# Optimization experiments

Measured on AMD Instinct MI355X. Metric: run time of the kernel, lower is better.

Reference implementation:

```python
import jax, jax.numpy as jnp
import numpy as np

N, E, H, C = 10000, 160000, 7, 64
NEG_SLOPE = 0.2


def setup_inputs() -> dict:
    key = jax.random.key(0)
    ks = iter(jax.random.split(key, 32))
    def w(shape, fan_in):
        return jax.random.normal(next(ks), shape, jnp.float32) * (1.0 / np.sqrt(fan_in))
    inp = {
        "x": jax.random.normal(next(ks), (N, 1024), jnp.float32),
        "edge_index": jax.random.randint(next(ks), (2, E), 0, N, jnp.int64),
        # input MLP 1024->512->256->64
        "W1": w((1024, 512), 1024), "b1": jnp.zeros((512,), jnp.float32),
        "W2": w((512, 256), 512),   "b2": jnp.zeros((256,), jnp.float32),
        "W3": w((256, 64), 256),    "b3": jnp.zeros((64,), jnp.float32),
        # 5 stacked GATv2Conv(64,64,heads=7,concat=False) layers
        "Wl": w((5, 64, H * C), 64), "bl": jnp.zeros((5, H * C), jnp.float32),
        "Wr": w((5, 64, H * C), 64),
        "att": w((5, H, C), C),
        "cbias": jnp.zeros((5, C), jnp.float32),
        # output MLP 64->32->16->9
        "V1": w((64, 32), 64), "c1": jnp.zeros((32,), jnp.float32),
        "V2": w((32, 16), 32), "c2": jnp.zeros((16,), jnp.float32),
        "V3": w((16, 9), 16),  "c3": jnp.zeros((9,), jnp.float32),
    }
    return inp


def _gatv2_conv(x, src, dst, Wl, bl, Wr, att, bias):
    # x: [N,64]; src/dst: [E'] (self-loops already appended)
    xl = (x @ Wl + bl).reshape(N, H, C)   # lin_l (with bias)
    xr = (x @ Wr).reshape(N, H, C)        # lin_r (no bias)
    e = jax.nn.leaky_relu(xl[src] + xr[dst], NEG_SLOPE)      # [E',H,C]
    logits = jnp.einsum('ehc,hc->eh', e, att)                # [E',H]
    m = jax.ops.segment_max(logits, dst, num_segments=N)     # [N,H]
    a = jnp.exp(logits - m[dst])
    s = jax.ops.segment_sum(a, dst, num_segments=N)          # [N,H]
    alpha = a / (s[dst] + 1e-16)                             # ragged softmax per dst node
    out = jax.ops.segment_sum(alpha[:, :, None] * xl[src], dst, num_segments=N)  # [N,H,C]
    return out.mean(axis=1) + bias                           # concat=False -> mean heads


def reference(x, edge_index, W1, b1, W2, b2, W3, b3, Wl, bl, Wr, att, cbias,
              V1, c1, V2, c2, V3, c3):
    # GATv2Conv adds self-loops by default
    loops = jnp.arange(N, dtype=edge_index.dtype)
    src = jnp.concatenate([edge_index[0], loops])
    dst = jnp.concatenate([edge_index[1], loops])

    h = jax.nn.relu(x @ W1 + b1)
    h = jax.nn.relu(h @ W2 + b2)
    h = jax.nn.relu(h @ W3 + b3)
    for l in range(5):
        h = jax.nn.relu(_gatv2_conv(h, src, dst, Wl[l], bl[l], Wr[l], att[l], cbias[l]))
    h = jax.nn.relu(h) @ V1 + c1
    h = jax.nn.relu(h) @ V2 + c2
    h = jax.nn.relu(h) @ V3 + c3
    return jax.nn.log_softmax(h, axis=1)
```

## Files before the change

### kernel.cpp

```cpp
#include <hip/hip_runtime.h>
#include <hip/hip_bf16.h>
#include <math.h>

#define NNODES 10000
#define NEDGES 160000
#define ETOT (NEDGES + NNODES)
#define HEADS 7
#define CH 64
#define HC 448
#define HCP 1024

typedef __attribute__((ext_vector_type(8))) short short8;
typedef __attribute__((ext_vector_type(4))) float floatx4;

__device__ __forceinline__ float bf_lo(unsigned u) {
  return __uint_as_float(u << 16);
}
__device__ __forceinline__ float bf_hi(unsigned u) {
  return __uint_as_float(u & 0xffff0000u);
}

__global__ __launch_bounds__(256) void convert_f32_bf16(
    const float* __restrict__ in, short* __restrict__ out, int n4) {
  int i = blockIdx.x * 256 + threadIdx.x;
  if (i < n4) {
    float4 v = *(const float4*)&in[(size_t)i * 4];
    short4 o;
    o.x = __bfloat16_as_short(__float2bfloat16(v.x));
    o.y = __bfloat16_as_short(__float2bfloat16(v.y));
    o.z = __bfloat16_as_short(__float2bfloat16(v.z));
    o.w = __bfloat16_as_short(__float2bfloat16(v.w));
    *(short4*)&out[(size_t)i * 4] = o;
  }
}

__global__ __launch_bounds__(256) void transpose_bf16(
    const float* __restrict__ in, short* __restrict__ out, int K, int N) {
  int idx = blockIdx.x * 256 + threadIdx.x;
  if (idx < K * N) {
    int n = idx / K, k = idx % K;
    out[idx] = __bfloat16_as_short(__float2bfloat16(in[(size_t)k * N + n]));
  }
}

__global__ __launch_bounds__(256) void pack_gat(
    const float* __restrict__ Wl, const float* __restrict__ Wr,
    const float* __restrict__ bl, short* __restrict__ Wgt,
    float* __restrict__ bg) {
  int idx = blockIdx.x * 256 + threadIdx.x;
  if (idx < 5 * HCP * 64) {
    int l = idx / (HCP * 64);
    int rem = idx % (HCP * 64);
    int col = rem / 64, k = rem % 64;
    int half = col >> 9;
    int within = col & 511;
    int c = within >> 3, h = within & 7;
    float v = 0.f;
    if (h < 7) {
      const float* W = half ? Wr : Wl;
      v = W[((size_t)l * 64 + k) * HC + h * 64 + c];
    }
    Wgt[idx] = __bfloat16_as_short(__float2bfloat16(v));
  }
  if (idx < 5 * HCP) {
    int l = idx >> 10, col = idx & 1023;
    int half = col >> 9, within = col & 511;
    int c = within >> 3, h = within & 7;
    bg[idx] = (!half && h < 7) ? bl[(size_t)l * HC + h * 64 + c] : 0.f;
  }
}

template <int BM, int BN, int RELU>
__global__ __launch_bounds__(256) void mfma_gemm(
    const short* __restrict__ A, const short* __restrict__ Bt,
    const float* __restrict__ bias, short* __restrict__ C,
    int M, int K, int Nc) {
  __shared__ short As[BM * 64];
  __shared__ short Bs[BN * 64];
  constexpr int MI = BM / 32;
  constexpr int NJ = BN / 32;
  int tid = threadIdx.x;
  int lane = tid & 63, wave = tid >> 6;
  int wm = wave >> 1, wn = wave & 1;
  int row0 = blockIdx.x * BM, col0 = blockIdx.y * BN;
  floatx4 acc[MI][NJ] = {};

  for (int k0 = 0; k0 < K; k0 += 64) {
    #pragma unroll
    for (int i = 0; i < BM / 32; ++i) {
      int c = i * 4 + wave;
      int r = c * 8 + (lane >> 3);
      int k = (lane & 7) * 8;
      int grow = row0 + r;
      if (grow >= M) grow = M - 1;
      __builtin_amdgcn_global_load_lds(
          (const __attribute__((address_space(1))) void*)(A + (size_t)grow * K + k0 + k),
          (__attribute__((address_space(3))) void*)(As + c * 512), 16, 0, 0);
    }
    #pragma unroll
    for (int i = 0; i < BN / 32; ++i) {
      int c = i * 4 + wave;
      int r = c * 8 + (lane >> 3);
      int k = (lane & 7) * 8;
      int gcol = col0 + r;
      if (gcol >= Nc) gcol = Nc - 1;
      __builtin_amdgcn_global_load_lds(
          (const __attribute__((address_space(1))) void*)(Bt + (size_t)gcol * K + k0 + k),
          (__attribute__((address_space(3))) void*)(Bs + c * 512), 16, 0, 0);
    }
    __syncthreads();
    int lr = lane & 15, lq = lane >> 4;
    #pragma unroll
    for (int kk = 0; kk < 64; kk += 32) {
      short8 af[MI], bf[NJ];
      #pragma unroll
      for (int i = 0; i < MI; ++i)
        af[i] = *(const short8*)&As[(wm * (BM / 2) + i * 16 + lr) * 64 + kk + lq * 8];
      #pragma unroll
      for (int j = 0; j < NJ; ++j)
        bf[j] = *(const short8*)&Bs[(wn * (BN / 2) + j * 16 + lr) * 64 + kk + lq * 8];
      #pragma unroll
      for (int i = 0; i < MI; ++i)
        #pragma unroll
        for (int j = 0; j < NJ; ++j)
          acc[i][j] = __builtin_amdgcn_mfma_f32_16x16x32_bf16(
              af[i], bf[j], acc[i][j], 0, 0, 0);
    }
    __syncthreads();
  }

  int lr = lane & 15, lq = lane >> 4;
  #pragma unroll
  for (int j = 0; j < NJ; ++j) {
    int col = col0 + wn * (BN / 2) + j * 16 + lr;
    float bj = bias ? bias[col] : 0.f;
    #pragma unroll
    for (int i = 0; i < MI; ++i) {
      int rbase = row0 + wm * (BM / 2) + i * 16 + lq * 4;
      #pragma unroll
      for (int r = 0; r < 4; ++r) {
        int row = rbase + r;
        if (row < M) {
          float v = acc[i][j][r] + bj;
          if (RELU) v = fmaxf(v, 0.f);
          C[(size_t)row * Nc + col] = __bfloat16_as_short(__float2bfloat16(v));
        }
      }
    }
  }
}

__global__ void init_cnt(int* __restrict__ cnt) {
  int i = blockIdx.x * 256 + threadIdx.x;
  if (i < NNODES) cnt[i] = 1;
}

__global__ void hist_kernel(const int* __restrict__ ei, int* __restrict__ cnt) {
  int e = blockIdx.x * 256 + threadIdx.x;
  if (e < NEDGES) atomicAdd(&cnt[ei[NEDGES + e]], 1);
}

__global__ __launch_bounds__(1024) void scan_kernel(
    const int* __restrict__ cnt, int* __restrict__ row_start,
    int* __restrict__ cursor) {
  __shared__ int wsum[16];
  int t = threadIdx.x;
  int lane = t & 63, w = t >> 6;
  int base = t * 10;
  int v[10], s = 0;
  #pragma unroll
  for (int i = 0; i < 10; ++i) {
    v[i] = (base + i < NNODES) ? cnt[base + i] : 0;
    s += v[i];
  }
  int incl = s;
  #pragma unroll
  for (int off = 1; off < 64; off <<= 1) {
    int o = __shfl_up(incl, off, 64);
    if (lane >= off) incl += o;
  }
  if (lane == 63) wsum[w] = incl;
  __syncthreads();
  if (w == 0) {
    int wv = (lane < 16) ? wsum[lane] : 0;
    #pragma unroll
    for (int off = 1; off < 16; off <<= 1) {
      int o = __shfl_up(wv, off, 64);
      if (lane >= off) wv += o;
    }
    if (lane < 16) wsum[lane] = wv;
  }
  __syncthreads();
  int woff = (w > 0) ? wsum[w - 1] : 0;
  int excl = woff + incl - s;
  #pragma unroll
  for (int i = 0; i < 10; ++i) {
    if (base + i < NNODES) {
      row_start[base + i] = excl;
      cursor[base + i] = excl;
    }
    excl += v[i];
  }
  if (t == 1023) row_start[NNODES] = wsum[15];
}

__global__ void scatter_self(int* __restrict__ cursor,
                             int* __restrict__ csr_src,
                             int* __restrict__ csr_dst) {
  int n = blockIdx.x * 256 + threadIdx.x;
  if (n < NNODES) {
    int pos = atomicAdd(&cursor[n], 1);
    csr_src[pos] = n;
    csr_dst[pos] = n;
  }
}

__global__ void scatter_kernel(const int* __restrict__ ei,
                               int* __restrict__ cursor,
                               int* __restrict__ csr_src,
                               int* __restrict__ csr_dst) {
  int e = blockIdx.x * 256 + threadIdx.x;
  if (e < NEDGES) {
    int d = ei[NEDGES + e];
    int pos = atomicAdd(&cursor[d], 1);
    csr_src[pos] = ei[e];
    csr_dst[pos] = d;
  }
}

__global__ __launch_bounds__(256) void edge_logits_kernel(
    const short* __restrict__ xlt, const float* __restrict__ att,
    const int* __restrict__ csr_src, const int* __restrict__ csr_dst,
    float* __restrict__ wbuf) {
  __shared__ float att_s[512];
  for (int i = threadIdx.x; i < 512; i += 256) {
    int c = i >> 3, h = i & 7;
    att_s[i] = (h < 7) ? att[h * 64 + c] : 0.f;
  }
  __syncthreads();
  int lane = threadIdx.x & 63;
  int wid = threadIdx.x >> 6;
  int eo = lane >> 3, cl = lane & 7;
  int e = (blockIdx.x * 4 + wid) * 8 + eo;
  int ec = (e < ETOT) ? e : (ETOT - 1);
  int s = csr_src[ec], d = csr_dst[ec];
  const uint4* xlp = (const uint4*)(xlt + (size_t)s * HCP);
  const uint4* xrp = (const uint4*)(xlt + (size_t)d * HCP + 512);
  float acc[7];
  #pragma unroll
  for (int h = 0; h < 7; ++h) acc[h] = 0.f;
  #pragma unroll
  for (int q = 0; q < 8; ++q) {
    int c = q * 8 + cl;
    uint4 a = xlp[c];
    uint4 b = xrp[c];
    float4 t0 = *(const float4*)&att_s[c * 8];
    float4 t1 = *(const float4*)&att_s[c * 8 + 4];
    float e0 = bf_lo(a.x) + bf_lo(b.x);
    float e1 = bf_hi(a.x) + bf_hi(b.x);
    float e2 = bf_lo(a.y) + bf_lo(b.y);
    float e3 = bf_hi(a.y) + bf_hi(b.y);
    float e4 = bf_lo(a.z) + bf_lo(b.z);
    float e5 = bf_hi(a.z) + bf_hi(b.z);
    float e6 = bf_lo(a.w) + bf_lo(b.w);
    e0 = fmaxf(e0, 0.2f * e0); e1 = fmaxf(e1, 0.2f * e1);
    e2 = fmaxf(e2, 0.2f * e2); e3 = fmaxf(e3, 0.2f * e3);
    e4 = fmaxf(e4, 0.2f * e4); e5 = fmaxf(e5, 0.2f * e5);
    e6 = fmaxf(e6, 0.2f * e6);
    acc[0] += t0.x * e0; acc[1] += t0.y * e1;
    acc[2] += t0.z * e2; acc[3] += t0.w * e3;
    acc[4] += t1.x * e4; acc[5] += t1.y * e5;
    acc[6] += t1.z * e6;
  }
  #pragma unroll
  for (int h = 0; h < 7; ++h) {
    acc[h] += __shfl_xor(acc[h], 1, 64);
    acc[h] += __shfl_xor(acc[h], 2, 64);
    acc[h] += __shfl_xor(acc[h], 4, 64);
  }
  float res = 0.f;
  #pragma unroll
  for (int h = 0; h < 7; ++h) res = (cl == h) ? acc[h] : res;
  float wv = (cl < 7) ? __expf(res) : 0.f;
  if (e < ETOT) wbuf[(size_t)e * 8 + cl] = wv;
}

__global__ __launch_bounds__(256) void gat_agg2_kernel(
    const short* __restrict__ xlt, const float* __restrict__ wbuf,
    const float* __restrict__ cbias, const int* __restrict__ row_start,
    const int* __restrict__ csr_src, short* __restrict__ hout) {
  int lane = threadIdx.x & 63;
  int wid = threadIdx.x >> 6;
  int n = blockIdx.x * 4 + wid;
  if (n >= NNODES) return;
  int beg = row_start[n], end = row_start[n + 1];

  float o0 = 0.f, o1 = 0.f, o2 = 0.f, o3 = 0.f, o4 = 0.f, o5 = 0.f, o6 = 0.f;
  float s0 = 0.f, s1 = 0.f, s2 = 0.f, s3 = 0.f, s4 = 0.f, s5 = 0.f, s6 = 0.f;
  #pragma unroll 2
  for (int e = beg; e < end; ++e) {
    int src = csr_src[e];
    float4 wa = *(const float4*)&wbuf[(size_t)e * 8];
    float4 wb = *(const float4*)&wbuf[(size_t)e * 8 + 4];
    uint4 xv = *(const uint4*)(xlt + (size_t)src * HCP + (size_t)lane * 8);
    o0 += wa.x * bf_lo(xv.x);
    o1 += wa.y * bf_hi(xv.x);
    o2 += wa.z * bf_lo(xv.y);
    o3 += wa.w * bf_hi(xv.y);
    o4 += wb.x * bf_lo(xv.z);
    o5 += wb.y * bf_hi(xv.z);
    o6 += wb.z * bf_lo(xv.w);
    s0 += wa.x; s1 += wa.y; s2 += wa.z; s3 += wa.w;
    s4 += wb.x; s5 += wb.y; s6 += wb.z;
  }

  float accv = o0 / (s0 + 1e-16f) + o1 / (s1 + 1e-16f) + o2 / (s2 + 1e-16f) +
               o3 / (s3 + 1e-16f) + o4 / (s4 + 1e-16f) + o5 / (s5 + 1e-16f) +
               o6 / (s6 + 1e-16f);
  float v = accv * (1.0f / 7.0f) + cbias[lane];
  hout[(size_t)n * 64 + lane] =
      __bfloat16_as_short(__float2bfloat16(fmaxf(v, 0.f)));
}

__global__ __launch_bounds__(256) void out_mlp_kernel(
    const short* __restrict__ h, const float* __restrict__ V1,
    const float* __restrict__ c1, const float* __restrict__ V2,
    const float* __restrict__ c2, const float* __restrict__ V3,
    const float* __restrict__ c3, float* __restrict__ out) {
  __shared__ float hb[4][64], r1[4][32], r2[4][16], z3[4][9];
  int wid = threadIdx.x >> 6;
  int t = threadIdx.x & 63;
  int n = blockIdx.x * 4 + wid;
  hb[wid][t] =
      __uint_as_float(((unsigned)((const unsigned short*)h)[(size_t)n * 64 + t]) << 16);
  __syncthreads();
  if (t < 32) {
    float a = c1[t];
    #pragma unroll
    for (int k = 0; k < 64; ++k) a += hb[wid][k] * V1[k * 32 + t];
    r1[wid][t] = fmaxf(a, 0.f);
  }
  __syncthreads();
  if (t < 16) {
    float a = c2[t];
    #pragma unroll
    for (int k = 0; k < 32; ++k) a += r1[wid][k] * V2[k * 16 + t];
    r2[wid][t] = fmaxf(a, 0.f);
  }
  __syncthreads();
  if (t < 9) {
    float a = c3[t];
    #pragma unroll
    for (int k = 0; k < 16; ++k) a += r2[wid][k] * V3[k * 9 + t];
    z3[wid][t] = a;
  }
  __syncthreads();
  if (t < 9) {
    float mx = z3[wid][0];
    #pragma unroll
    for (int k = 1; k < 9; ++k) mx = fmaxf(mx, z3[wid][k]);
    float s = 0.f;
    #pragma unroll
    for (int k = 0; k < 9; ++k) s += __expf(z3[wid][k] - mx);
    out[(size_t)n * 9 + t] = z3[wid][t] - mx - logf(s);
  }
}

extern "C" void kernel_launch(void* const* d_in, const int* in_sizes, int n_in,
                              void* d_out, int out_size, void* d_ws, size_t ws_size,
                              hipStream_t stream) {
  const float* x   = (const float*)d_in[0];
  const int*   ei  = (const int*)d_in[1];
  const float* W1  = (const float*)d_in[2];
  const float* b1  = (const float*)d_in[3];
  const float* W2  = (const float*)d_in[4];
  const float* b2  = (const float*)d_in[5];
  const float* W3  = (const float*)d_in[6];
  const float* b3  = (const float*)d_in[7];
  const float* Wl  = (const float*)d_in[8];
  const float* bl  = (const float*)d_in[9];
  const float* Wr  = (const float*)d_in[10];
  const float* att = (const float*)d_in[11];
  const float* cb  = (const float*)d_in[12];
  const float* V1  = (const float*)d_in[13];
  const float* c1  = (const float*)d_in[14];
  const float* V2  = (const float*)d_in[15];
  const float* c2  = (const float*)d_in[16];
  const float* V3  = (const float*)d_in[17];
  const float* c3  = (const float*)d_in[18];
  float* out = (float*)d_out;

  char* ws = (char*)d_ws;
  size_t off = 0;
  auto alloc = [&](size_t bytes) {
    void* p = ws + off;
    off = (off + bytes + 255) & ~(size_t)255;
    return p;
  };
  char* region0 = (char*)alloc((size_t)NNODES * 1024 * 2 + 1024);
  short* xb  = (short*)region0;
  short* h2  = (short*)region0;
  short* xlt = (short*)region0;
  char* region1 = (char*)alloc((size_t)NNODES * 512 * 2 + 1024);
  short* h1 = (short*)region1;
  short* hA = (short*)region1;
  short* hB = hA + (size_t)NNODES * 64;
  short* W1t = (short*)alloc((size_t)512 * 1024 * 2);
  short* W2t = (short*)alloc((size_t)256 * 512 * 2);
  short* W3t = (short*)alloc((size_t)64 * 256 * 2);
  short* Wgt = (short*)alloc((size_t)5 * HCP * 64 * 2);
  float* bg  = (float*)alloc((size_t)5 * HCP * 4);
  int* cnt       = (int*)alloc((size_t)NNODES * 4);
  int* row_start = (int*)alloc((size_t)(NNODES + 1) * 4);
  int* cursor    = (int*)alloc((size_t)NNODES * 4);
  int* csr_src   = (int*)alloc((size_t)ETOT * 4);
  int* csr_dst   = (int*)alloc((size_t)ETOT * 4);
  float* wbuf    = (float*)alloc((size_t)ETOT * 8 * 4);

  convert_f32_bf16<<<(NNODES * 1024 / 4 + 255) / 256, 256, 0, stream>>>(
      x, xb, NNODES * 1024 / 4);
  transpose_bf16<<<(1024 * 512 + 255) / 256, 256, 0, stream>>>(W1, W1t, 1024, 512);
  transpose_bf16<<<(512 * 256 + 255) / 256, 256, 0, stream>>>(W2, W2t, 512, 256);
  transpose_bf16<<<(256 * 64 + 255) / 256, 256, 0, stream>>>(W3, W3t, 256, 64);
  pack_gat<<<(5 * HCP * 64 + 255) / 256, 256, 0, stream>>>(Wl, Wr, bl, Wgt, bg);

  init_cnt<<<(NNODES + 255) / 256, 256, 0, stream>>>(cnt);
  hist_kernel<<<(NEDGES + 255) / 256, 256, 0, stream>>>(ei, cnt);
  scan_kernel<<<1, 1024, 0, stream>>>(cnt, row_start, cursor);
  scatter_self<<<(NNODES + 255) / 256, 256, 0, stream>>>(cursor, csr_src, csr_dst);
  scatter_kernel<<<(NEDGES + 255) / 256, 256, 0, stream>>>(ei, cursor, csr_src, csr_dst);

  mfma_gemm<64, 128, 1><<<dim3(157, 4), 256, 0, stream>>>(
      xb, W1t, b1, h1, NNODES, 1024, 512);
  mfma_gemm<64, 128, 1><<<dim3(157, 2), 256, 0, stream>>>(
      h1, W2t, b2, h2, NNODES, 512, 256);
  mfma_gemm<64, 64, 1><<<dim3(157, 1), 256, 0, stream>>>(
      h2, W3t, b3, hA, NNODES, 256, 64);

  short* hcur = hA;
  short* hnext = hB;
  for (int layer = 0; layer < 5; ++layer) {
    mfma_gemm<128, 128, 0><<<dim3(79, 8), 256, 0, stream>>>(
        hcur, Wgt + (size_t)layer * HCP * 64, bg + (size_t)layer * HCP, xlt,
        NNODES, 64, HCP);
    edge_logits_kernel<<<(ETOT + 31) / 32, 256, 0, stream>>>(
        xlt, att + (size_t)layer * HC, csr_src, csr_dst, wbuf);
    gat_agg2_kernel<<<2500, 256, 0, stream>>>(
        xlt, wbuf, cb + (size_t)layer * 64, row_start, csr_src, hnext);
    short* tmp = hcur; hcur = hnext; hnext = tmp;
  }

  out_mlp_kernel<<<2500, 256, 0, stream>>>(hcur, V1, c1, V2, c2, V3, c3, out);
}
```

Baseline: 579.8 us.

## Merge prep kernels, fuse self-loop scatter, split aggregation, fuse output MLP

Folds the input conversion, the weight transposes, the GAT weight packing and the count init into a single prep kernel. It also merges the self-loop scatter into the edge scatter kernel. The GAT aggregation now uses two waves per destination node, each taking alternate edges, with partial sums reduced through shared memory. The output MLP and log-softmax are fused into the final layer's aggregation kernel. The goal is fewer kernel launches and more parallelism per node, at the cost of an extra barrier, shared-memory traffic and half the waves idling during the epilogue.

```diff
diff --git a/kernel.cpp b/kernel.cpp
--- a/kernel.cpp
+++ b/kernel.cpp
@@ -19,38 +19,49 @@
 __device__ __forceinline__ float bf_hi(unsigned u) {
   return __uint_as_float(u & 0xffff0000u);
 }
-
-__global__ __launch_bounds__(256) void convert_f32_bf16(
-    const float* __restrict__ in, short* __restrict__ out, int n4) {
-  int i = blockIdx.x * 256 + threadIdx.x;
-  if (i < n4) {
-    float4 v = *(const float4*)&in[(size_t)i * 4];
-    short4 o;
-    o.x = __bfloat16_as_short(__float2bfloat16(v.x));
-    o.y = __bfloat16_as_short(__float2bfloat16(v.y));
-    o.z = __bfloat16_as_short(__float2bfloat16(v.z));
-    o.w = __bfloat16_as_short(__float2bfloat16(v.w));
-    *(short4*)&out[(size_t)i * 4] = o;
-  }
-}
-
-__global__ __launch_bounds__(256) void transpose_bf16(
-    const float* __restrict__ in, short* __restrict__ out, int K, int N) {
-  int idx = blockIdx.x * 256 + threadIdx.x;
-  if (idx < K * N) {
-    int n = idx / K, k = idx % K;
-    out[idx] = __bfloat16_as_short(__float2bfloat16(in[(size_t)k * N + n]));
-  }
-}
-
-__global__ __launch_bounds__(256) void pack_gat(
+__device__ __forceinline__ short f2bf(float v) {
+  return __bfloat16_as_short(__float2bfloat16(v));
+}
+
+#define P0 2560000
+#define P1 (P0 + 512 * 1024)
+#define P2 (P1 + 256 * 512)
+#define P3 (P2 + 64 * 256)
+#define P4 (P3 + 5 * HCP * 64)
+#define P5 (P4 + 5 * HCP)
+#define P6 (P5 + NNODES)
+#define PTOT P6
+
+__global__ __launch_bounds__(256) void prep_kernel(
+    const float* __restrict__ x, short* __restrict__ xb,
+    const float* __restrict__ W1, short* __restrict__ W1t,
+    const float* __restrict__ W2, short* __restrict__ W2t,
+    const float* __restrict__ W3, short* __restrict__ W3t,
     const float* __restrict__ Wl, const float* __restrict__ Wr,
     const float* __restrict__ bl, short* __restrict__ Wgt,
-    float* __restrict__ bg) {
+    float* __restrict__ bg, int* __restrict__ cnt) {
   int idx = blockIdx.x * 256 + threadIdx.x;
-  if (idx < 5 * HCP * 64) {
-    int l = idx / (HCP * 64);
-    int rem = idx % (HCP * 64);
+  if (idx < P0) {
+    float4 v = *(const float4*)&x[(size_t)idx * 4];
+    short4 o;
+    o.x = f2bf(v.x); o.y = f2bf(v.y); o.z = f2bf(v.z); o.w = f2bf(v.w);
+    *(short4*)&xb[(size_t)idx * 4] = o;
+  } else if (idx < P1) {
+    int i = idx - P0;
+    int n = i / 1024, k = i % 1024;
+    W1t[i] = f2bf(W1[(size_t)k * 512 + n]);
+  } else if (idx < P2) {
+    int i = idx - P1;
+    int n = i / 512, k = i % 512;
+    W2t[i] = f2bf(W2[(size_t)k * 256 + n]);
+  } else if (idx < P3) {
+    int i = idx - P2;
+    int n = i / 256, k = i % 256;
+    W3t[i] = f2bf(W3[(size_t)k * 64 + n]);
+  } else if (idx < P4) {
+    int i = idx - P3;
+    int l = i / (HCP * 64);
+    int rem = i % (HCP * 64);
     int col = rem / 64, k = rem % 64;
     int half = col >> 9;
     int within = col & 511;
@@ -60,13 +71,15 @@
       const float* W = half ? Wr : Wl;
       v = W[((size_t)l * 64 + k) * HC + h * 64 + c];
     }
-    Wgt[idx] = __bfloat16_as_short(__float2bfloat16(v));
-  }
-  if (idx < 5 * HCP) {
-    int l = idx >> 10, col = idx & 1023;
+    Wgt[i] = f2bf(v);
+  } else if (idx < P5) {
+    int i = idx - P4;
+    int l = i >> 10, col = i & 1023;
     int half = col >> 9, within = col & 511;
     int c = within >> 3, h = within & 7;
-    bg[idx] = (!half && h < 7) ? bl[(size_t)l * HC + h * 64 + c] : 0.f;
+    bg[i] = (!half && h < 7) ? bl[(size_t)l * HC + h * 64 + c] : 0.f;
+  } else if (idx < P6) {
+    cnt[idx - P5] = 1;
   }
 }
 
@@ -143,16 +156,11 @@
         if (row < M) {
           float v = acc[i][j][r] + bj;
           if (RELU) v = fmaxf(v, 0.f);
-          C[(size_t)row * Nc + col] = __bfloat16_as_short(__float2bfloat16(v));
+          C[(size_t)row * Nc + col] = f2bf(v);
         }
       }
     }
   }
-}
-
-__global__ void init_cnt(int* __restrict__ cnt) {
-  int i = blockIdx.x * 256 + threadIdx.x;
-  if (i < NNODES) cnt[i] = 1;
 }
 
 __global__ void hist_kernel(const int* __restrict__ ei, int* __restrict__ cnt) {
@@ -204,23 +212,17 @@
   if (t == 1023) row_start[NNODES] = wsum[15];
 }
 
-__global__ void scatter_self(int* __restrict__ cursor,
-                             int* __restrict__ csr_src,
-                             int* __restrict__ csr_dst) {
-  int n = blockIdx.x * 256 + threadIdx.x;
-  if (n < NNODES) {
-    int pos = atomicAdd(&cursor[n], 1);
-    csr_src[pos] = n;
-    csr_dst[pos] = n;
-  }
-}
-
 __global__ void scatter_kernel(const int* __restrict__ ei,
                                int* __restrict__ cursor,
                                int* __restrict__ csr_src,
                                int* __restrict__ csr_dst) {
-  int e = blockIdx.x * 256 + threadIdx.x;
-  if (e < NEDGES) {
+  int t = blockIdx.x * 256 + threadIdx.x;
+  if (t < NNODES) {
+    int pos = atomicAdd(&cursor[t], 1);
+    csr_src[pos] = t;
+    csr_dst[pos] = t;
+  } else if (t < ETOT) {
+    int e = t - NNODES;
     int d = ei[NEDGES + e];
     int pos = atomicAdd(&cursor[d], 1);
     csr_src[pos] = ei[e];
@@ -285,20 +287,28 @@
   if (e < ETOT) wbuf[(size_t)e * 8 + cl] = wv;
 }
 
+template <int FINAL>
 __global__ __launch_bounds__(256) void gat_agg2_kernel(
     const short* __restrict__ xlt, const float* __restrict__ wbuf,
     const float* __restrict__ cbias, const int* __restrict__ row_start,
-    const int* __restrict__ csr_src, short* __restrict__ hout) {
+    const int* __restrict__ csr_src, short* __restrict__ hout,
+    const float* __restrict__ V1, const float* __restrict__ c1,
+    const float* __restrict__ V2, const float* __restrict__ c2,
+    const float* __restrict__ V3, const float* __restrict__ c3,
+    float* __restrict__ out) {
+  __shared__ float part[2][14][64];
+  __shared__ float hb[2][64], r1[2][32], r2[2][16], z3[2][9];
   int lane = threadIdx.x & 63;
-  int wid = threadIdx.x >> 6;
-  int n = blockIdx.x * 4 + wid;
-  if (n >= NNODES) return;
+  int wv = threadIdx.x >> 6;
+  int nw = wv >> 1;
+  int half = wv & 1;
+  int n = blockIdx.x * 2 + nw;
   int beg = row_start[n], end = row_start[n + 1];
 
   float o0 = 0.f, o1 = 0.f, o2 = 0.f, o3 = 0.f, o4 = 0.f, o5 = 0.f, o6 = 0.f;
   float s0 = 0.f, s1 = 0.f, s2 = 0.f, s3 = 0.f, s4 = 0.f, s5 = 0.f, s6 = 0.f;
   #pragma unroll 2
-  for (int e = beg; e < end; ++e) {
+  for (int e = beg + half; e < end; e += 2) {
     int src = csr_src[e];
     float4 wa = *(const float4*)&wbuf[(size_t)e * 8];
     float4 wb = *(const float4*)&wbuf[(size_t)e * 8 + 4];
@@ -314,55 +324,63 @@
     s4 += wb.x; s5 += wb.y; s6 += wb.z;
   }
 
-  float accv = o0 / (s0 + 1e-16f) + o1 / (s1 + 1e-16f) + o2 / (s2 + 1e-16f) +
-               o3 / (s3 + 1e-16f) + o4 / (s4 + 1e-16f) + o5 / (s5 + 1e-16f) +
-               o6 / (s6 + 1e-16f);
-  float v = accv * (1.0f / 7.0f) + cbias[lane];
-  hout[(size_t)n * 64 + lane] =
-      __bfloat16_as_short(__float2bfloat16(fmaxf(v, 0.f)));
-}
-
-__global__ __launch_bounds__(256) void out_mlp_kernel(
-    const short* __restrict__ h, const float* __restrict__ V1,
-    const float* __restrict__ c1, const float* __restrict__ V2,
-    const float* __restrict__ c2, const float* __restrict__ V3,
-    const float* __restrict__ c3, float* __restrict__ out) {
-  __shared__ float hb[4][64], r1[4][32], r2[4][16], z3[4][9];
-  int wid = threadIdx.x >> 6;
-  int t = threadIdx.x & 63;
-  int n = blockIdx.x * 4 + wid;
-  hb[wid][t] =
-      __uint_as_float(((unsigned)((const unsigned short*)h)[(size_t)n * 64 + t]) << 16);
+  if (half == 1) {
+    part[nw][0][lane] = o0;  part[nw][1][lane] = o1;
+    part[nw][2][lane] = o2;  part[nw][3][lane] = o3;
+    part[nw][4][lane] = o4;  part[nw][5][lane] = o5;
+    part[nw][6][lane] = o6;
+    part[nw][7][lane] = s0;  part[nw][8][lane] = s1;
+    part[nw][9][lane] = s2;  part[nw][10][lane] = s3;
+    part[nw][11][lane] = s4; part[nw][12][lane] = s5;
+    part[nw][13][lane] = s6;
+  }
   __syncthreads();
-  if (t < 32) {
-    float a = c1[t];
-    #pragma unroll
-    for (int k = 0; k < 64; ++k) a += hb[wid][k] * V1[k * 32 + t];
-    r1[wid][t] = fmaxf(a, 0.f);
-  }
-  __syncthreads();
-  if (t < 16) {
-    float a = c2[t];
-    #pragma unroll
-    for (int k = 0; k < 32; ++k) a += r1[wid][k] * V2[k * 16 + t];
-    r2[wid][t] = fmaxf(a, 0.f);
-  }
-  __syncthreads();
-  if (t < 9) {
-    float a = c3[t];
-    #pragma unroll
-    for (int k = 0; k < 16; ++k) a += r2[wid][k] * V3[k * 9 + t];
-    z3[wid][t] = a;
-  }
-  __syncthreads();
-  if (t < 9) {
-    float mx = z3[wid][0];
-    #pragma unroll
-    for (int k = 1; k < 9; ++k) mx = fmaxf(mx, z3[wid][k]);
-    float s = 0.f;
-    #pragma unroll
-    for (int k = 0; k < 9; ++k) s += __expf(z3[wid][k] - mx);
-    out[(size_t)n * 9 + t] = z3[wid][t] - mx - logf(s);
+  if (half == 0) {
+    o0 += part[nw][0][lane];  o1 += part[nw][1][lane];
+    o2 += part[nw][2][lane];  o3 += part[nw][3][lane];
+    o4 += part[nw][4][lane];  o5 += part[nw][5][lane];
+    o6 += part[nw][6][lane];
+    s0 += part[nw][7][lane];  s1 += part[nw][8][lane];
+    s2 += part[nw][9][lane];  s3 += part[nw][10][lane];
+    s4 += part[nw][11][lane]; s5 += part[nw][12][lane];
+    s6 += part[nw][13][lane];
+    float accv = o0 / (s0 + 1e-16f) + o1 / (s1 + 1e-16f) + o2 / (s2 + 1e-16f) +
+                 o3 / (s3 + 1e-16f) + o4 / (s4 + 1e-16f) + o5 / (s5 + 1e-16f) +
+                 o6 / (s6 + 1e-16f);
+    float v = fmaxf(accv * (1.0f / 7.0f) + cbias[lane], 0.f);
+    if (!FINAL) {
+      hout[(size_t)n * 64 + lane] = f2bf(v);
+    } else {
+      int t = lane;
+      hb[nw][t] = v;
+      if (t < 32) {
+        float a = c1[t];
+        #pragma unroll
+        for (int k = 0; k < 64; ++k) a += hb[nw][k] * V1[k * 32 + t];
+        r1[nw][t] = fmaxf(a, 0.f);
+      }
+      if (t < 16) {
+        float a = c2[t];
+        #pragma unroll
+        for (int k = 0; k < 32; ++k) a += r1[nw][k] * V2[k * 16 + t];
+        r2[nw][t] = fmaxf(a, 0.f);
+      }
+      if (t < 9) {
+        float a = c3[t];
+        #pragma unroll
+        for (int k = 0; k < 16; ++k) a += r2[nw][k] * V3[k * 9 + t];
+        z3[nw][t] = a;
+      }
+      if (t < 9) {
+        float mx = z3[nw][0];
+        #pragma unroll
+        for (int k = 1; k < 9; ++k) mx = fmaxf(mx, z3[nw][k]);
+        float s = 0.f;
+        #pragma unroll
+        for (int k = 0; k < 9; ++k) s += __expf(z3[nw][k] - mx);
+        out[(size_t)n * 9 + t] = z3[nw][t] - mx - logf(s);
+      }
+    }
   }
 }
 
@@ -417,18 +435,12 @@
   int* csr_dst   = (int*)alloc((size_t)ETOT * 4);
   float* wbuf    = (float*)alloc((size_t)ETOT * 8 * 4);
 
-  convert_f32_bf16<<<(NNODES * 1024 / 4 + 255) / 256, 256, 0, stream>>>(
-      x, xb, NNODES * 1024 / 4);
-  transpose_bf16<<<(1024 * 512 + 255) / 256, 256, 0, stream>>>(W1, W1t, 1024, 512);
-  transpose_bf16<<<(512 * 256 + 255) / 256, 256, 0, stream>>>(W2, W2t, 512, 256);
-  transpose_bf16<<<(256 * 64 + 255) / 256, 256, 0, stream>>>(W3, W3t, 256, 64);
-  pack_gat<<<(5 * HCP * 64 + 255) / 256, 256, 0, stream>>>(Wl, Wr, bl, Wgt, bg);
-
-  init_cnt<<<(NNODES + 255) / 256, 256, 0, stream>>>(cnt);
+  prep_kernel<<<(PTOT + 255) / 256, 256, 0, stream>>>(
+      x, xb, W1, W1t, W2, W2t, W3, W3t, Wl, Wr, bl, Wgt, bg, cnt);
+
   hist_kernel<<<(NEDGES + 255) / 256, 256, 0, stream>>>(ei, cnt);
   scan_kernel<<<1, 1024, 0, stream>>>(cnt, row_start, cursor);
-  scatter_self<<<(NNODES + 255) / 256, 256, 0, stream>>>(cursor, csr_src, csr_dst);
-  scatter_kernel<<<(NEDGES + 255) / 256, 256, 0, stream>>>(ei, cursor, csr_src, csr_dst);
+  scatter_kernel<<<(ETOT + 255) / 256, 256, 0, stream>>>(ei, cursor, csr_src, csr_dst);
 
   mfma_gemm<64, 128, 1><<<dim3(157, 4), 256, 0, stream>>>(
       xb, W1t, b1, h1, NNODES, 1024, 512);
@@ -445,10 +457,15 @@
         NNODES, 64, HCP);
     edge_logits_kernel<<<(ETOT + 31) / 32, 256, 0, stream>>>(
         xlt, att + (size_t)layer * HC, csr_src, csr_dst, wbuf);
-    gat_agg2_kernel<<<2500, 256, 0, stream>>>(
-        xlt, wbuf, cb + (size_t)layer * 64, row_start, csr_src, hnext);
+    if (layer < 4) {
+      gat_agg2_kernel<0><<<5000, 256, 0, stream>>>(
+          xlt, wbuf, cb + (size_t)layer * 64, row_start, csr_src, hnext,
+          V1, c1, V2, c2, V3, c3, out);
+    } else {
+      gat_agg2_kernel<1><<<5000, 256, 0, stream>>>(
+          xlt, wbuf, cb + (size_t)layer * 64, row_start, csr_src, hnext,
+          V1, c1, V2, c2, V3, c3, out);
+    }
     short* tmp = hcur; hcur = hnext; hnext = tmp;
   }
-
-  out_mlp_kernel<<<2500, 256, 0, stream>>>(hcur, V1, c1, V2, c2, V3, c3, out);
-}
+}
```

Result: faster. 551.7 us (-4.8%).
